# Kernel optimization log

Measured on AMD Instinct MI355X. Metric: run time of the kernel, lower is better.

## Reference

```python
import jax, jax.numpy as jnp
import numpy as np

N = 50000
E = 800000
IN_F, HID, OUT_F = 512, 256, 64
KEEP = 0.5  # Dropout(0.5)


def setup_inputs() -> dict:
    key = jax.random.key(0)
    ks = jax.random.split(key, 7)
    X = jax.random.normal(ks[0], (N, IN_F), dtype=jnp.float32)
    # Xavier-uniform-style init for the two layer weights
    lim1 = float(np.sqrt(6.0 / (IN_F + HID)))
    lim2 = float(np.sqrt(6.0 / (HID + OUT_F)))
    W1 = jax.random.uniform(ks[1], (IN_F, HID), jnp.float32, -lim1, lim1)
    W2 = jax.random.uniform(ks[2], (HID, OUT_F), jnp.float32, -lim2, lim2)
    a_row = jnp.sort(jax.random.randint(ks[3], (E,), 0, N)).astype(jnp.int64)
    a_col = jax.random.randint(ks[4], (E,), 0, N).astype(jnp.int64)
    a_val = jax.random.uniform(ks[5], (E,), jnp.float32)
    drop_mask = jax.random.randint(ks[6], (N, HID), 0, 2).astype(jnp.int32)
    return {"X": X, "W1": W1, "W2": W2, "a_row": a_row, "a_col": a_col,
            "a_val": a_val, "drop_mask": drop_mask}


def _spmm(a_row, a_col, a_val, dense):
    # A @ dense where A is [N, N] sparse in COO form: gather + weighted segment-sum
    msgs = a_val[:, None] * dense[a_col]          # [E, d]
    return jax.ops.segment_sum(msgs, a_row, num_segments=N)


def reference(X, W1, W2, a_row, a_col, a_val, drop_mask):
    # layer 1: feature transform + neighbor aggregation
    h = _spmm(a_row, a_col, a_val, X @ W1)        # [N, HID]
    h = jax.nn.relu(h)
    h = h * drop_mask.astype(h.dtype) * (1.0 / KEEP)  # Dropout(0.5), train mode
    # layer 2
    out = _spmm(a_row, a_col, a_val, h @ W2)      # [N, OUT_F]
    return jax.nn.log_softmax(out, axis=1)
```

## Files before the change

### kernel.cpp

```cpp
#include <hip/hip_runtime.h>
#include <hip/hip_bf16.h>
#include <math.h>

#define NN   50000
#define EE   800000
#define INF  512
#define HIDF 256
#define OUTF 64
#define MTILES (NN/16)

using short8 = __attribute__((ext_vector_type(8))) short;
using short4v = __attribute__((ext_vector_type(4))) short;
using f32x4  = __attribute__((ext_vector_type(4))) float;

static __device__ __forceinline__ short f2bf(float f){
  unsigned u = __builtin_bit_cast(unsigned, f);
  u += 0x7fff + ((u >> 16) & 1);
  return (short)(u >> 16);
}
static __device__ __forceinline__ float bf2f(short s){
  unsigned u = ((unsigned)(unsigned short)s) << 16;
  return __builtin_bit_cast(float, u);
}

__global__ void k_prep(const int* __restrict__ a_row, int* __restrict__ row_ptr,
                       const float* __restrict__ W1, short* __restrict__ W1p,
                       const float* __restrict__ W2, short* __restrict__ W2bT){
  int b = blockIdx.x, tid = threadIdx.x;
  if (b < 196){
    int i = b * 256 + tid;
    if (i > NN) return;
    int lo = 0, hi = EE;
    while (lo < hi){ int mid = (lo + hi) >> 1; if (a_row[mid] < i) lo = mid + 1; else hi = mid; }
    row_ptr[i] = lo;
  } else if (b < 708){
    int idx = (b - 196) * 256 + tid;
    int k = idx >> 8, col = idx & 255;
    int kk = k >> 5, k2 = k & 31;
    W1p[((kk << 8) + col) * 32 + k2] = f2bf(W1[idx]);
  } else {
    int idx = (b - 708) * 256 + tid;
    int k = idx >> 6, n = idx & 63;
    W2bT[n * HIDF + k] = f2bf(W2[idx]);
  }
}

__global__ __launch_bounds__(256) void k_gemm1(const float* __restrict__ X,
                                               const short* __restrict__ W1p,
                                               short* __restrict__ XW1b){
  __shared__ short lds[256 * 40];
  int wave = threadIdx.x >> 6, lane = threadIdx.x & 63;
  int l16 = lane & 15, quad = lane >> 4;
  int m0 = blockIdx.x * 128 + wave * 32;
  int r0 = min(m0 + l16, NN - 1);
  int r1 = min(m0 + 16 + l16, NN - 1);
  const float* arow0 = X + (size_t)r0 * INF + quad * 8;
  const float* arow1 = X + (size_t)r1 * INF + quad * 8;

  f32x4 acc0[16], acc1[16];
  #pragma unroll
  for (int t = 0; t < 16; t++){ acc0[t] = (f32x4){0.f,0.f,0.f,0.f}; acc1[t] = (f32x4){0.f,0.f,0.f,0.f}; }

  for (int kk = 0; kk < INF/32; kk++){
    const float4* ap0 = (const float4*)(arow0 + kk * 32);
    const float4* ap1 = (const float4*)(arow1 + kk * 32);
    float4 a00 = ap0[0], a01 = ap0[1];
    float4 a10 = ap1[0], a11 = ap1[1];

    const short* chunk = W1p + kk * (256*32);
    #pragma unroll
    for (int j = 0; j < 4; j++){
      int off16 = j * 256 + threadIdx.x;
      int col = off16 >> 2, kq = threadIdx.x & 3;
      *(short8*)(lds + col * 40 + kq * 8) = *(const short8*)(chunk + off16 * 8);
    }
    __syncthreads();

    short8 af0, af1;
    af0[0]=f2bf(a00.x); af0[1]=f2bf(a00.y); af0[2]=f2bf(a00.z); af0[3]=f2bf(a00.w);
    af0[4]=f2bf(a01.x); af0[5]=f2bf(a01.y); af0[6]=f2bf(a01.z); af0[7]=f2bf(a01.w);
    af1[0]=f2bf(a10.x); af1[1]=f2bf(a10.y); af1[2]=f2bf(a10.z); af1[3]=f2bf(a10.w);
    af1[4]=f2bf(a11.x); af1[5]=f2bf(a11.y); af1[6]=f2bf(a11.z); af1[7]=f2bf(a11.w);
    #pragma unroll
    for (int nt = 0; nt < 16; nt++){
      short8 bf = *(const short8*)(lds + (nt*16 + l16) * 40 + quad * 8);
      acc0[nt] = __builtin_amdgcn_mfma_f32_16x16x32_bf16(af0, bf, acc0[nt], 0, 0, 0);
      acc1[nt] = __builtin_amdgcn_mfma_f32_16x16x32_bf16(af1, bf, acc1[nt], 0, 0, 0);
    }
    __syncthreads();
  }
  #pragma unroll
  for (int nt = 0; nt < 16; nt++){
    int col = nt*16 + l16;
    #pragma unroll
    for (int r = 0; r < 4; r++){
      int row0 = m0 + quad*4 + r;
      int row1 = m0 + 16 + quad*4 + r;
      if (row0 < NN) XW1b[(size_t)row0 * HIDF + col] = f2bf(acc0[nt][r]);
      if (row1 < NN) XW1b[(size_t)row1 * HIDF + col] = f2bf(acc1[nt][r]);
    }
  }
}

__global__ __launch_bounds__(256) void k_spmm1(const int* __restrict__ row_ptr,
                                               const int* __restrict__ a_col,
                                               const float* __restrict__ a_val,
                                               const short* __restrict__ XW1b,
                                               const int* __restrict__ drop_mask,
                                               short* __restrict__ hb){
  int wave = threadIdx.x >> 6, lane = threadIdx.x & 63;
  int r = blockIdx.x * 4 + wave;
  int s = row_ptr[r], e = row_ptr[r+1];
  int g = lane >> 4;
  int c16 = lane & 15;
  float acc[16];
  #pragma unroll
  for (int j = 0; j < 16; j++) acc[j] = 0.f;

  int i = s + g;
  for (; i + 4 < e; i += 8){
    float v0 = a_val[i];     int c0 = a_col[i];
    float v1 = a_val[i+4];   int c1 = a_col[i+4];
    const short* p0 = XW1b + (size_t)c0 * HIDF + c16 * 16;
    const short* p1 = XW1b + (size_t)c1 * HIDF + c16 * 16;
    short8 x0a = *(const short8*)(p0);
    short8 x0b = *(const short8*)(p0 + 8);
    short8 x1a = *(const short8*)(p1);
    short8 x1b = *(const short8*)(p1 + 8);
    #pragma unroll
    for (int j = 0; j < 8; j++){
      acc[j]   += v0 * bf2f(x0a[j]);  acc[j+8] += v0 * bf2f(x0b[j]);
      acc[j]   += v1 * bf2f(x1a[j]);  acc[j+8] += v1 * bf2f(x1b[j]);
    }
  }
  for (; i < e; i += 4){
    float v = a_val[i];  int c = a_col[i];
    const short* p = XW1b + (size_t)c * HIDF + c16 * 16;
    short8 xa = *(const short8*)(p);
    short8 xb = *(const short8*)(p + 8);
    #pragma unroll
    for (int j = 0; j < 8; j++){
      acc[j] += v * bf2f(xa[j]);  acc[j+8] += v * bf2f(xb[j]);
    }
  }
  #pragma unroll
  for (int j = 0; j < 16; j++){
    acc[j] += __shfl_xor(acc[j], 16);
    acc[j] += __shfl_xor(acc[j], 32);
  }
  if (lane < 16){
    const int* dm = drop_mask + (size_t)r * HIDF + c16 * 16;
    short8 o0, o1;
    #pragma unroll
    for (int j = 0; j < 8; j++){
      o0[j] = f2bf(fmaxf(acc[j],   0.f) * (float)dm[j]   * 2.0f);
      o1[j] = f2bf(fmaxf(acc[j+8], 0.f) * (float)dm[j+8] * 2.0f);
    }
    short* hp = hb + (size_t)r * HIDF + c16 * 16;
    *(short8*)(hp)     = o0;
    *(short8*)(hp + 8) = o1;
  }
}

__global__ __launch_bounds__(256) void k_gemm2(const short* __restrict__ A,
                                               const short* __restrict__ BT,
                                               short* __restrict__ C){
  int wave = threadIdx.x >> 6, lane = threadIdx.x & 63;
  int tile_m = blockIdx.x * 4 + wave;
  if (tile_m >= MTILES) return;
  int m0 = tile_m * 16, l16 = lane & 15, quad = lane >> 4;

  f32x4 acc[4];
  #pragma unroll
  for (int t = 0; t < 4; t++) acc[t] = (f32x4){0.f,0.f,0.f,0.f};

  const short* ar = A + (size_t)(m0 + l16) * HIDF + quad * 8;
  for (int kk = 0; kk < HIDF/32; kk++){
    short8 af = *(const short8*)(ar + kk * 32);
    #pragma unroll
    for (int nt = 0; nt < 4; nt++){
      short8 bf = *(const short8*)(BT + (size_t)(nt*16 + l16) * HIDF + kk*32 + quad*8);
      acc[nt] = __builtin_amdgcn_mfma_f32_16x16x32_bf16(af, bf, acc[nt], 0, 0, 0);
    }
  }
  #pragma unroll
  for (int nt = 0; nt < 4; nt++){
    int col = nt*16 + l16;
    #pragma unroll
    for (int r = 0; r < 4; r++)
      C[(size_t)(m0 + quad*4 + r) * OUTF + col] = f2bf(acc[nt][r]);
  }
}

__global__ __launch_bounds__(256) void k_spmm2_lsm(const int* __restrict__ row_ptr,
                                                   const int* __restrict__ a_col,
                                                   const float* __restrict__ a_val,
                                                   const short* __restrict__ HW2b,
                                                   float* __restrict__ out){
  int wave = threadIdx.x >> 6, lane = threadIdx.x & 63;
  int r = blockIdx.x * 4 + wave;
  int s = row_ptr[r], e = row_ptr[r+1];
  int g = lane >> 4;
  int c4 = lane & 15;
  float acc[4] = {0,0,0,0};

  int i = s + g;
  for (; i + 4 < e; i += 8){
    float v0 = a_val[i];    int c0 = a_col[i];
    float v1 = a_val[i+4];  int c1 = a_col[i+4];
    short4v x0 = *(const short4v*)(HW2b + (size_t)c0 * OUTF + c4 * 4);
    short4v x1 = *(const short4v*)(HW2b + (size_t)c1 * OUTF + c4 * 4);
    #pragma unroll
    for (int j = 0; j < 4; j++){ acc[j] += v0 * bf2f(x0[j]); acc[j] += v1 * bf2f(x1[j]); }
  }
  for (; i < e; i += 4){
    float v = a_val[i];  int c = a_col[i];
    short4v x = *(const short4v*)(HW2b + (size_t)c * OUTF + c4 * 4);
    #pragma unroll
    for (int j = 0; j < 4; j++) acc[j] += v * bf2f(x[j]);
  }
  #pragma unroll
  for (int j = 0; j < 4; j++){
    acc[j] += __shfl_xor(acc[j], 16);
    acc[j] += __shfl_xor(acc[j], 32);
  }
  float m = fmaxf(fmaxf(acc[0], acc[1]), fmaxf(acc[2], acc[3]));
  #pragma unroll
  for (int o = 1; o <= 8; o <<= 1) m = fmaxf(m, __shfl_xor(m, o));
  float ssum = expf(acc[0]-m) + expf(acc[1]-m) + expf(acc[2]-m) + expf(acc[3]-m);
  #pragma unroll
  for (int o = 1; o <= 8; o <<= 1) ssum += __shfl_xor(ssum, o);
  float ls = logf(ssum);
  if (lane < 16){
    float4 o4 = { acc[0]-m-ls, acc[1]-m-ls, acc[2]-m-ls, acc[3]-m-ls };
    *(float4*)(out + (size_t)r * OUTF + c4 * 4) = o4;
  }
}

extern "C" void kernel_launch(void* const* d_in, const int* in_sizes, int n_in,
                              void* d_out, int out_size, void* d_ws, size_t ws_size,
                              hipStream_t stream) {
  const float* X      = (const float*)d_in[0];
  const float* W1     = (const float*)d_in[1];
  const float* W2     = (const float*)d_in[2];
  const int*   a_row  = (const int*)d_in[3];
  const int*   a_col  = (const int*)d_in[4];
  const float* a_val  = (const float*)d_in[5];
  const int*   drop   = (const int*)d_in[6];
  float*       out    = (float*)d_out;

  char* ws = (char*)d_ws;
  int*   row_ptr = (int*)  (ws);
  short* W1p     = (short*)(ws + 200704);
  short* W2bT    = (short*)(ws + 462848);
  short* XW1b    = (short*)(ws + 495616);
  short* hb      = (short*)(ws + 26095616);
  short* HW2b    = (short*)(ws + 51695616);

  k_prep<<<772, 256, 0, stream>>>(a_row, row_ptr, W1, W1p, W2, W2bT);
  k_gemm1<<<(NN + 127)/128, 256, 0, stream>>>(X, W1p, XW1b);
  k_spmm1<<<NN/4, 256, 0, stream>>>(row_ptr, a_col, a_val, XW1b, drop, hb);
  k_gemm2<<<(MTILES + 3)/4, 256, 0, stream>>>(hb, W2bT, HW2b);
  k_spmm2_lsm<<<NN/4, 256, 0, stream>>>(row_ptr, a_col, a_val, HW2b, out);
}
```

Measured before the change: 336.7 us.

## Drop LDS staging in gemm1 and widen per-lane gathers in both SpMMs

```diff
diff --git a/kernel.cpp b/kernel.cpp
--- a/kernel.cpp
+++ b/kernel.cpp
@@ -45,13 +45,12 @@
   }
 }
 
-__global__ __launch_bounds__(256) void k_gemm1(const float* __restrict__ X,
+__global__ __launch_bounds__(128) void k_gemm1(const float* __restrict__ X,
                                                const short* __restrict__ W1p,
                                                short* __restrict__ XW1b){
-  __shared__ short lds[256 * 40];
   int wave = threadIdx.x >> 6, lane = threadIdx.x & 63;
   int l16 = lane & 15, quad = lane >> 4;
-  int m0 = blockIdx.x * 128 + wave * 32;
+  int m0 = blockIdx.x * 64 + wave * 32;
   int r0 = min(m0 + l16, NN - 1);
   int r1 = min(m0 + 16 + l16, NN - 1);
   const float* arow0 = X + (size_t)r0 * INF + quad * 8;
@@ -66,28 +65,19 @@
     const float4* ap1 = (const float4*)(arow1 + kk * 32);
     float4 a00 = ap0[0], a01 = ap0[1];
     float4 a10 = ap1[0], a11 = ap1[1];
-
-    const short* chunk = W1p + kk * (256*32);
-    #pragma unroll
-    for (int j = 0; j < 4; j++){
-      int off16 = j * 256 + threadIdx.x;
-      int col = off16 >> 2, kq = threadIdx.x & 3;
-      *(short8*)(lds + col * 40 + kq * 8) = *(const short8*)(chunk + off16 * 8);
-    }
-    __syncthreads();
-
     short8 af0, af1;
     af0[0]=f2bf(a00.x); af0[1]=f2bf(a00.y); af0[2]=f2bf(a00.z); af0[3]=f2bf(a00.w);
     af0[4]=f2bf(a01.x); af0[5]=f2bf(a01.y); af0[6]=f2bf(a01.z); af0[7]=f2bf(a01.w);
     af1[0]=f2bf(a10.x); af1[1]=f2bf(a10.y); af1[2]=f2bf(a10.z); af1[3]=f2bf(a10.w);
     af1[4]=f2bf(a11.x); af1[5]=f2bf(a11.y); af1[6]=f2bf(a11.z); af1[7]=f2bf(a11.w);
+
+    const short* bchunk = W1p + kk * (256*32);
     #pragma unroll
     for (int nt = 0; nt < 16; nt++){
-      short8 bf = *(const short8*)(lds + (nt*16 + l16) * 40 + quad * 8);
+      short8 bf = *(const short8*)(bchunk + (nt*16 + l16) * 32 + quad * 8);
       acc0[nt] = __builtin_amdgcn_mfma_f32_16x16x32_bf16(af0, bf, acc0[nt], 0, 0, 0);
       acc1[nt] = __builtin_amdgcn_mfma_f32_16x16x32_bf16(af1, bf, acc1[nt], 0, 0, 0);
     }
-    __syncthreads();
   }
   #pragma unroll
   for (int nt = 0; nt < 16; nt++){
@@ -111,54 +101,58 @@
   int wave = threadIdx.x >> 6, lane = threadIdx.x & 63;
   int r = blockIdx.x * 4 + wave;
   int s = row_ptr[r], e = row_ptr[r+1];
-  int g = lane >> 4;
-  int c16 = lane & 15;
-  float acc[16];
-  #pragma unroll
-  for (int j = 0; j < 16; j++) acc[j] = 0.f;
+  int g = lane >> 3;
+  int c8 = lane & 7;
+  float acc[32];
+  #pragma unroll
+  for (int j = 0; j < 32; j++) acc[j] = 0.f;
 
   int i = s + g;
-  for (; i + 4 < e; i += 8){
+  for (; i + 8 < e; i += 16){
     float v0 = a_val[i];     int c0 = a_col[i];
-    float v1 = a_val[i+4];   int c1 = a_col[i+4];
-    const short* p0 = XW1b + (size_t)c0 * HIDF + c16 * 16;
-    const short* p1 = XW1b + (size_t)c1 * HIDF + c16 * 16;
-    short8 x0a = *(const short8*)(p0);
-    short8 x0b = *(const short8*)(p0 + 8);
-    short8 x1a = *(const short8*)(p1);
-    short8 x1b = *(const short8*)(p1 + 8);
-    #pragma unroll
-    for (int j = 0; j < 8; j++){
-      acc[j]   += v0 * bf2f(x0a[j]);  acc[j+8] += v0 * bf2f(x0b[j]);
-      acc[j]   += v1 * bf2f(x1a[j]);  acc[j+8] += v1 * bf2f(x1b[j]);
-    }
-  }
-  for (; i < e; i += 4){
+    float v1 = a_val[i+8];   int c1 = a_col[i+8];
+    const short* p0 = XW1b + (size_t)c0 * HIDF + c8 * 32;
+    const short* p1 = XW1b + (size_t)c1 * HIDF + c8 * 32;
+    short8 x0[4], x1[4];
+    #pragma unroll
+    for (int q = 0; q < 4; q++){ x0[q] = *(const short8*)(p0 + q*8); }
+    #pragma unroll
+    for (int q = 0; q < 4; q++){ x1[q] = *(const short8*)(p1 + q*8); }
+    #pragma unroll
+    for (int q = 0; q < 4; q++)
+      #pragma unroll
+      for (int j = 0; j < 8; j++){
+        acc[q*8+j] += v0 * bf2f(x0[q][j]);
+        acc[q*8+j] += v1 * bf2f(x1[q][j]);
+      }
+  }
+  for (; i < e; i += 8){
     float v = a_val[i];  int c = a_col[i];
-    const short* p = XW1b + (size_t)c * HIDF + c16 * 16;
-    short8 xa = *(const short8*)(p);
-    short8 xb = *(const short8*)(p + 8);
-    #pragma unroll
-    for (int j = 0; j < 8; j++){
-      acc[j] += v * bf2f(xa[j]);  acc[j+8] += v * bf2f(xb[j]);
-    }
-  }
-  #pragma unroll
-  for (int j = 0; j < 16; j++){
+    const short* p = XW1b + (size_t)c * HIDF + c8 * 32;
+    #pragma unroll
+    for (int q = 0; q < 4; q++){
+      short8 x = *(const short8*)(p + q*8);
+      #pragma unroll
+      for (int j = 0; j < 8; j++) acc[q*8+j] += v * bf2f(x[j]);
+    }
+  }
+  #pragma unroll
+  for (int j = 0; j < 32; j++){
+    acc[j] += __shfl_xor(acc[j], 8);
     acc[j] += __shfl_xor(acc[j], 16);
     acc[j] += __shfl_xor(acc[j], 32);
   }
-  if (lane < 16){
-    const int* dm = drop_mask + (size_t)r * HIDF + c16 * 16;
-    short8 o0, o1;
-    #pragma unroll
-    for (int j = 0; j < 8; j++){
-      o0[j] = f2bf(fmaxf(acc[j],   0.f) * (float)dm[j]   * 2.0f);
-      o1[j] = f2bf(fmaxf(acc[j+8], 0.f) * (float)dm[j+8] * 2.0f);
-    }
-    short* hp = hb + (size_t)r * HIDF + c16 * 16;
-    *(short8*)(hp)     = o0;
-    *(short8*)(hp + 8) = o1;
+  if (lane < 8){
+    const int* dm = drop_mask + (size_t)r * HIDF + c8 * 32;
+    short* hp = hb + (size_t)r * HIDF + c8 * 32;
+    #pragma unroll
+    for (int q = 0; q < 4; q++){
+      short8 o;
+      #pragma unroll
+      for (int j = 0; j < 8; j++)
+        o[j] = f2bf(fmaxf(acc[q*8+j], 0.f) * (float)dm[q*8+j] * 2.0f);
+      *(short8*)(hp + q*8) = o;
+    }
   }
 }
 
@@ -200,40 +194,50 @@
   int wave = threadIdx.x >> 6, lane = threadIdx.x & 63;
   int r = blockIdx.x * 4 + wave;
   int s = row_ptr[r], e = row_ptr[r+1];
-  int g = lane >> 4;
-  int c4 = lane & 15;
-  float acc[4] = {0,0,0,0};
+  int g = lane >> 3;
+  int c8 = lane & 7;
+  float acc[8];
+  #pragma unroll
+  for (int j = 0; j < 8; j++) acc[j] = 0.f;
 
   int i = s + g;
-  for (; i + 4 < e; i += 8){
+  for (; i + 8 < e; i += 16){
     float v0 = a_val[i];    int c0 = a_col[i];
-    float v1 = a_val[i+4];  int c1 = a_col[i+4];
-    short4v x0 = *(const short4v*)(HW2b + (size_t)c0 * OUTF + c4 * 4);
-    short4v x1 = *(const short4v*)(HW2b + (size_t)c1 * OUTF + c4 * 4);
-    #pragma unroll
-    for (int j = 0; j < 4; j++){ acc[j] += v0 * bf2f(x0[j]); acc[j] += v1 * bf2f(x1[j]); }
-  }
-  for (; i < e; i += 4){
+    float v1 = a_val[i+8];  int c1 = a_col[i+8];
+    short8 x0 = *(const short8*)(HW2b + (size_t)c0 * OUTF + c8 * 8);
+    short8 x1 = *(const short8*)(HW2b + (size_t)c1 * OUTF + c8 * 8);
+    #pragma unroll
+    for (int j = 0; j < 8; j++){ acc[j] += v0 * bf2f(x0[j]); acc[j] += v1 * bf2f(x1[j]); }
+  }
+  for (; i < e; i += 8){
     float v = a_val[i];  int c = a_col[i];
-    short4v x = *(const short4v*)(HW2b + (size_t)c * OUTF + c4 * 4);
-    #pragma unroll
-    for (int j = 0; j < 4; j++) acc[j] += v * bf2f(x[j]);
-  }
-  #pragma unroll
-  for (int j = 0; j < 4; j++){
+    short8 x = *(const short8*)(HW2b + (size_t)c * OUTF + c8 * 8);
+    #pragma unroll
+    for (int j = 0; j < 8; j++) acc[j] += v * bf2f(x[j]);
+  }
+  #pragma unroll
+  for (int j = 0; j < 8; j++){
+    acc[j] += __shfl_xor(acc[j], 8);
     acc[j] += __shfl_xor(acc[j], 16);
     acc[j] += __shfl_xor(acc[j], 32);
   }
-  float m = fmaxf(fmaxf(acc[0], acc[1]), fmaxf(acc[2], acc[3]));
-  #pragma unroll
-  for (int o = 1; o <= 8; o <<= 1) m = fmaxf(m, __shfl_xor(m, o));
-  float ssum = expf(acc[0]-m) + expf(acc[1]-m) + expf(acc[2]-m) + expf(acc[3]-m);
-  #pragma unroll
-  for (int o = 1; o <= 8; o <<= 1) ssum += __shfl_xor(ssum, o);
+  float m = acc[0];
+  #pragma unroll
+  for (int j = 1; j < 8; j++) m = fmaxf(m, acc[j]);
+  #pragma unroll
+  for (int o = 1; o <= 4; o <<= 1) m = fmaxf(m, __shfl_xor(m, o));
+  float ssum = 0.f;
+  #pragma unroll
+  for (int j = 0; j < 8; j++) ssum += expf(acc[j] - m);
+  #pragma unroll
+  for (int o = 1; o <= 4; o <<= 1) ssum += __shfl_xor(ssum, o);
   float ls = logf(ssum);
-  if (lane < 16){
-    float4 o4 = { acc[0]-m-ls, acc[1]-m-ls, acc[2]-m-ls, acc[3]-m-ls };
-    *(float4*)(out + (size_t)r * OUTF + c4 * 4) = o4;
+  if (lane < 8){
+    float4 o0 = { acc[0]-m-ls, acc[1]-m-ls, acc[2]-m-ls, acc[3]-m-ls };
+    float4 o1 = { acc[4]-m-ls, acc[5]-m-ls, acc[6]-m-ls, acc[7]-m-ls };
+    float* op = out + (size_t)r * OUTF + c8 * 8;
+    *(float4*)(op)     = o0;
+    *(float4*)(op + 4) = o1;
   }
 }
 
@@ -258,7 +262,7 @@
   short* HW2b    = (short*)(ws + 51695616);
 
   k_prep<<<772, 256, 0, stream>>>(a_row, row_ptr, W1, W1p, W2, W2bT);
-  k_gemm1<<<(NN + 127)/128, 256, 0, stream>>>(X, W1p, XW1b);
+  k_gemm1<<<(NN + 63)/64, 128, 0, stream>>>(X, W1p, XW1b);
   k_spmm1<<<NN/4, 256, 0, stream>>>(row_ptr, a_col, a_val, XW1b, drop, hb);
   k_gemm2<<<(MTILES + 3)/4, 256, 0, stream>>>(hb, W2bT, HW2b);
   k_spmm2_lsm<<<NN/4, 256, 0, stream>>>(row_ptr, a_col, a_val, HW2b, out);
```

Measured after the change: 355.6 us. +5.6%, slower.
